# Kernel optimization log

Measured on AMD Instinct MI355X. Metric: run time of the kernel, lower is better.

Reference implementation:

```python
import jax, jax.numpy as jnp
import numpy as np

B, N, C, H = 2, 2048, 1024, 16
D = C // H
NEG = -1e9  # keras Softmax large negative for masked positions


def setup_inputs() -> dict:
    key = jax.random.key(0)
    ks = jax.random.split(key, 10)
    s = lambda fan_in: 1.0 / np.sqrt(fan_in)
    return {
        "x": jax.random.normal(ks[0], (B, N, C), jnp.float32),
        "mask": jnp.ones((B, 1, 1, N), jnp.bool_),
        "Wqkv": jax.random.normal(ks[1], (C, 3 * C), jnp.float32) * s(C),
        "bqkv": jnp.zeros((3 * C,), jnp.float32),
        "Wl": jax.random.normal(ks[2], (H, H), jnp.float32) * s(H),
        "bl": jnp.zeros((H,), jnp.float32),
        "Ww": jax.random.normal(ks[3], (H, H), jnp.float32) * s(H),
        "bw": jnp.zeros((H,), jnp.float32),
        "Wp": jax.random.normal(ks[4], (C, C), jnp.float32) * s(C),
        "bp": jnp.zeros((C,), jnp.float32),
    }


def reference(x, mask, Wqkv, bqkv, Wl, bl, Ww, bw, Wp, bp):
    scale = jnp.asarray(D ** -0.5, x.dtype)
    qkv = x @ Wqkv + bqkv                                  # [B,N,3C]
    qkv = qkv.reshape(B, N, 3, H, D).transpose(2, 0, 3, 1, 4)  # [3,B,H,N,D]
    q, k, v = qkv[0] * scale, qkv[1], qkv[2]
    attn = jnp.einsum("bhnd,bhmd->bhnm", q, k)             # [B,H,N,N]
    # pre-softmax talking-heads: mix head axis
    attn = jnp.einsum("bhnm,hg->bgnm", attn, Wl) + bl[None, :, None, None]
    # keras Softmax with boolean mask: add -1e9 where mask is False
    attn = attn + (1.0 - mask.astype(attn.dtype)) * NEG
    attn = jax.nn.softmax(attn, axis=-1)
    # post-softmax talking-heads
    attn = jnp.einsum("bhnm,hg->bgnm", attn, Ww) + bw[None, :, None, None]
    out = jnp.einsum("bhnm,bhmd->bhnd", attn, v)           # [B,H,N,D]
    out = out.transpose(0, 2, 1, 3).reshape(B, N, C)
    return out @ Wp + bp
```

## Files before the change

kernel.cpp:

```cpp
#include <hip/hip_runtime.h>
#include <hip/hip_bf16.h>


typedef __bf16 bf16_t;
typedef __bf16 bf16x8 __attribute__((ext_vector_type(8)));
typedef float f32x4 __attribute__((ext_vector_type(4)));

#define DEV static __device__ __forceinline__

static constexpr float NEGV = -1e9f;

DEV f32x4 mfma16(bf16x8 a, bf16x8 b, f32x4 c) {
  return __builtin_amdgcn_mfma_f32_16x16x32_bf16(a, b, c, 0, 0, 0);
}

DEV bf16x8 zero8() {
  bf16x8 z;
#pragma unroll
  for (int j = 0; j < 8; ++j) z[j] = (bf16_t)0.0f;
  return z;
}

DEV uint32_t pkbf(float lo, float hi) {
  union { bf16_t f; unsigned short s; } a, b;
  a.f = (bf16_t)lo; b.f = (bf16_t)hi;
  return (uint32_t)a.s | ((uint32_t)b.s << 16);
}

union U84 { uint32_t u[4]; bf16x8 v; };

__global__ __launch_bounds__(256) void mask_prep(const unsigned char* __restrict__ raw,
                                                 unsigned char* __restrict__ canon) {
  __shared__ int c0, c12;
  const int tid = threadIdx.x;
  if (tid == 0) { c0 = 0; c12 = 0; }
  __syncthreads();
  int l0 = 0, l12 = 0;
  for (int i = tid; i < 4096; i += 256) {
    unsigned char v = raw[i];
    if (v) {
      int r = i & 3;
      if (r == 0) l0++;
      else if (r < 3) l12++;
    }
  }
  if (l0) atomicAdd(&c0, l0);
  if (l12) atomicAdd(&c12, l12);
  __syncthreads();
  const int mode = (c0 == 0) ? 2 : ((c12 > 0) ? 0 : 1);
  for (int i = tid; i < 4096; i += 256) {
    bool t;
    if (mode == 0)      t = raw[i] != 0;
    else if (mode == 1) t = ((const int*)raw)[i] != 0;
    else                t = ((const float*)raw)[i] != 0.0f;
    canon[i] = t ? 1 : 0;
  }
}

__global__ __launch_bounds__(256) void gemm_kernel(
    const float* __restrict__ Af, const bf16_t* __restrict__ Ab,
    const float* __restrict__ Bw, const float* __restrict__ bias,
    float* __restrict__ outf,
    bf16_t* __restrict__ Qs, bf16_t* __restrict__ Ks, bf16_t* __restrict__ Vt,
    int K, int Nn, int epi) {
  __shared__ bf16_t As[64][40];
  __shared__ bf16_t Bs[64][40];
  const int tid = threadIdx.x;
  const int lane = tid & 63, wid = tid >> 6;
  const int bx = blockIdx.x, by = blockIdx.y;
  const int wr = (wid >> 1) * 32, wc = (wid & 1) * 32;
  const int lr = lane & 15, kq = lane >> 4;

  f32x4 acc[2][2];
#pragma unroll
  for (int i = 0; i < 2; ++i)
#pragma unroll
    for (int j = 0; j < 2; ++j) acc[i][j] = (f32x4){0.f, 0.f, 0.f, 0.f};

  for (int kt = 0; kt < K; kt += 32) {
    {
      const int row = tid >> 2, c8 = (tid & 3) * 8;
      if (epi == 0) {
        const float* p = Af + (size_t)(bx * 64 + row) * K + kt + c8;
        float4 v0 = *(const float4*)p;
        float4 v1 = *(const float4*)(p + 4);
        bf16x8 v;
        v[0] = (bf16_t)v0.x; v[1] = (bf16_t)v0.y; v[2] = (bf16_t)v0.z; v[3] = (bf16_t)v0.w;
        v[4] = (bf16_t)v1.x; v[5] = (bf16_t)v1.y; v[6] = (bf16_t)v1.z; v[7] = (bf16_t)v1.w;
        *(bf16x8*)&As[row][c8] = v;
      } else {
        *(bf16x8*)&As[row][c8] =
            *(const bf16x8*)(Ab + (size_t)(bx * 64 + row) * K + kt + c8);
      }
      const int krow = tid >> 3, n8 = (tid & 7) * 8;
      const float* bp = Bw + (size_t)(kt + krow) * Nn + by * 64 + n8;
      float4 b0 = *(const float4*)bp;
      float4 b1 = *(const float4*)(bp + 4);
      Bs[n8 + 0][krow] = (bf16_t)b0.x; Bs[n8 + 1][krow] = (bf16_t)b0.y;
      Bs[n8 + 2][krow] = (bf16_t)b0.z; Bs[n8 + 3][krow] = (bf16_t)b0.w;
      Bs[n8 + 4][krow] = (bf16_t)b1.x; Bs[n8 + 5][krow] = (bf16_t)b1.y;
      Bs[n8 + 6][krow] = (bf16_t)b1.z; Bs[n8 + 7][krow] = (bf16_t)b1.w;
    }
    __syncthreads();
#pragma unroll
    for (int rt = 0; rt < 2; ++rt) {
      bf16x8 af = *(const bf16x8*)&As[wr + rt * 16 + lr][kq * 8];
#pragma unroll
      for (int ct = 0; ct < 2; ++ct) {
        bf16x8 bf = *(const bf16x8*)&Bs[wc + ct * 16 + lr][kq * 8];
        acc[rt][ct] = mfma16(af, bf, acc[rt][ct]);
      }
    }
    __syncthreads();
  }

#pragma unroll
  for (int rt = 0; rt < 2; ++rt)
#pragma unroll
    for (int ct = 0; ct < 2; ++ct)
#pragma unroll
      for (int r = 0; r < 4; ++r) {
        const int grow = bx * 64 + wr + rt * 16 + kq * 4 + r;
        const int gcol = by * 64 + wc + ct * 16 + lr;
        const float v = acc[rt][ct][r] + bias[gcol];
        if (epi == 0) {
          const int t = gcol >> 10, h = (gcol >> 6) & 15, d = gcol & 63;
          const int b = grow >> 11, n = grow & 2047;
          if (t == 0)
            Qs[(((size_t)b * 16 + h) * 2048 + n) * 64 + d] = (bf16_t)(v * 0.125f);
          else if (t == 1)
            Ks[(((size_t)b * 16 + h) * 2048 + n) * 64 + d] = (bf16_t)v;
          else
            Vt[(((size_t)b * 16 + h) * 64 + d) * 2048 + n] = (bf16_t)v;
        } else {
          outf[(size_t)grow * Nn + gcol] = v;
        }
      }
}

__global__ __launch_bounds__(256) void vsum_kernel(const bf16_t* __restrict__ Vt,
                                                   float* __restrict__ Vsum) {
  const int lane = threadIdx.x & 63, wid = threadIdx.x >> 6;
  const int row = blockIdx.x * 4 + wid;
  const bf16_t* p = Vt + (size_t)row * 2048;
  float s = 0.f;
#pragma unroll
  for (int it = 0; it < 4; ++it) {
    bf16x8 v = *(const bf16x8*)(p + it * 512 + lane * 8);
#pragma unroll
    for (int j = 0; j < 8; ++j) s += (float)v[j];
  }
#pragma unroll
  for (int off = 32; off; off >>= 1) s += __shfl_xor(s, off);
  if (lane == 0) Vsum[row] = s;
}

__global__ __launch_bounds__(512, 4) void attn_pass1(
    const bf16_t* __restrict__ Qs, const bf16_t* __restrict__ Ks,
    const unsigned char* __restrict__ canon,
    const float* __restrict__ Wl, const float* __restrict__ bl,
    float2* __restrict__ pstats) {
  __shared__ uint32_t SE[512 * 10];
  const int tid = threadIdx.x, lane = tid & 63, wid = tid >> 6;
  const int g = lane & 15, kq = lane >> 4;
  const int b = blockIdx.z, n0 = blockIdx.x * 16, mbeg = blockIdx.y * 1024;
  const int h0 = wid * 2;

  bf16x8 wlf;
#pragma unroll
  for (int j = 0; j < 8; ++j) {
    const int k = kq * 8 + j;
    wlf[j] = (k < 16) ? (bf16_t)Wl[k * 16 + g] : (bf16_t)0.0f;
  }
  const float blg = bl[g];

  bf16x8 qf[2][2];
#pragma unroll
  for (int hh = 0; hh < 2; ++hh)
#pragma unroll
    for (int ks = 0; ks < 2; ++ks)
      qf[hh][ks] = *(const bf16x8*)(Qs + (((size_t)b * 16 + h0 + hh) * 2048 +
                                          n0 + g) * 64 + ks * 32 + kq * 8);

  float run_m[2] = {-3e38f, -3e38f}, run_l[2] = {0.f, 0.f};

  for (int m0 = mbeg; m0 < mbeg + 1024; m0 += 32) {
#pragma unroll
    for (int mt = 0; mt < 2; ++mt) {
      f32x4 a[2];
#pragma unroll
      for (int hh = 0; hh < 2; ++hh) {
        const bf16_t* kp = Ks + (((size_t)b * 16 + h0 + hh) * 2048 + m0 +
                                 mt * 16 + g) * 64 + kq * 8;
        a[hh] = mfma16(qf[hh][0], *(const bf16x8*)kp, (f32x4){0.f, 0.f, 0.f, 0.f});
        a[hh] = mfma16(qf[hh][1], *(const bf16x8*)(kp + 32), a[hh]);
      }
#pragma unroll
      for (int r = 0; r < 4; ++r) {
        const int p = (kq * 4 + r) * 32 + mt * 16 + g;
        SE[p * 10 + (wid ^ (kq & 1))] = pkbf(a[0][r], a[1][r]);
      }
    }
    __syncthreads();
#pragma unroll
    for (int pp = 0; pp < 4; ++pp) {
      const int pg = wid * 4 + pp, nl = pp >> 1, mt = pg & 1;
      const int prow = pg * 16 + g, bp = (prow >> 7) & 1;
      bf16x8 sf;
      if (kq < 2) {
        U84 t;
#pragma unroll
        for (int i = 0; i < 4; ++i) t.u[i] = SE[prow * 10 + ((kq * 4 + i) ^ bp)];
        sf = t.v;
      } else sf = zero8();
      f32x4 sp = mfma16(sf, wlf, (f32x4){blg, blg, blg, blg});
      const uchar4 mk = *(const uchar4*)(canon + b * 2048 + m0 + mt * 16 + kq * 4);
      if (!mk.x) sp[0] += NEGV;
      if (!mk.y) sp[1] += NEGV;
      if (!mk.z) sp[2] += NEGV;
      if (!mk.w) sp[3] += NEGV;
      float tm = fmaxf(fmaxf(sp[0], sp[1]), fmaxf(sp[2], sp[3]));
      tm = fmaxf(tm, __shfl_xor(tm, 16));
      tm = fmaxf(tm, __shfl_xor(tm, 32));
      const float nm = fmaxf(run_m[nl], tm);
      float s = __expf(sp[0] - nm) + __expf(sp[1] - nm) +
                __expf(sp[2] - nm) + __expf(sp[3] - nm);
      s += __shfl_xor(s, 16);
      s += __shfl_xor(s, 32);
      run_l[nl] = run_l[nl] * __expf(run_m[nl] - nm) + s;
      run_m[nl] = nm;
    }
    __syncthreads();
  }
  if (kq == 0) {
#pragma unroll
    for (int i = 0; i < 2; ++i) {
      const int n = n0 + wid * 2 + i;
      pstats[(((size_t)b * 2 + blockIdx.y) * 2048 + n) * 16 + g] =
          make_float2(run_m[i], run_l[i]);
    }
  }
}

__global__ __launch_bounds__(256) void stats_merge(const float2* __restrict__ ps,
                                                   float2* __restrict__ fin) {
  const int i = blockIdx.x * 256 + threadIdx.x;
  const int b = i >> 15, rest = i & 32767;
  const float2 p0 = ps[((size_t)b * 2 + 0) * 32768 + rest];
  const float2 p1 = ps[((size_t)b * 2 + 1) * 32768 + rest];
  const float M = fmaxf(p0.x, p1.x);
  const float L = p0.y * __expf(p0.x - M) + p1.y * __expf(p1.x - M);
  fin[i] = make_float2(M, 1.0f / L);
}

__global__ __launch_bounds__(512, 4) void attn_pass2(
    const bf16_t* __restrict__ Qs, const bf16_t* __restrict__ Ks,
    const bf16_t* __restrict__ Vt, const unsigned char* __restrict__ canon,
    const float* __restrict__ Wl, const float* __restrict__ bl,
    const float* __restrict__ Ww, const float2* __restrict__ fin2,
    float* __restrict__ Opart) {
  __shared__ uint32_t SE[512 * 10];
  __shared__ uint32_t Fw[16 * 324];
  const int tid = threadIdx.x, lane = tid & 63, wid = tid >> 6;
  const int g = lane & 15, kq = lane >> 4;
  const int b = blockIdx.z, n0 = blockIdx.x * 16, mbeg = blockIdx.y * 1024;
  const int h0 = wid * 2;

  bf16x8 wlf, wwt;
#pragma unroll
  for (int j = 0; j < 8; ++j) {
    const int k = kq * 8 + j;
    wlf[j] = (k < 16) ? (bf16_t)Wl[k * 16 + g] : (bf16_t)0.0f;
    wwt[j] = (k < 16) ? (bf16_t)Ww[k * 16 + g] : (bf16_t)0.0f;
  }
  f32x4 blv;
#pragma unroll
  for (int r = 0; r < 4; ++r) blv[r] = bl[kq * 4 + r];

  bf16x8 qf[2][2];
#pragma unroll
  for (int hh = 0; hh < 2; ++hh)
#pragma unroll
    for (int ks = 0; ks < 2; ++ks)
      qf[hh][ks] = *(const bf16x8*)(Qs + (((size_t)b * 16 + h0 + hh) * 2048 +
                                          n0 + g) * 64 + ks * 32 + kq * 8);

  f32x4 oacc[2][4];
#pragma unroll
  for (int i = 0; i < 2; ++i)
#pragma unroll
    for (int j = 0; j < 4; ++j) oacc[i][j] = (f32x4){0.f, 0.f, 0.f, 0.f};

  for (int m0 = mbeg; m0 < mbeg + 1024; m0 += 32) {
#pragma unroll
    for (int mt = 0; mt < 2; ++mt) {
      f32x4 a[2];
#pragma unroll
      for (int hh = 0; hh < 2; ++hh) {
        const bf16_t* kp = Ks + (((size_t)b * 16 + h0 + hh) * 2048 + m0 +
                                 mt * 16 + g) * 64 + kq * 8;
        a[hh] = mfma16(qf[hh][0], *(const bf16x8*)kp, (f32x4){0.f, 0.f, 0.f, 0.f});
        a[hh] = mfma16(qf[hh][1], *(const bf16x8*)(kp + 32), a[hh]);
      }
#pragma unroll
      for (int r = 0; r < 4; ++r) {
        const int p = (kq * 4 + r) * 32 + mt * 16 + g;
        SE[p * 10 + (wid ^ (kq & 1))] = pkbf(a[0][r], a[1][r]);
      }
    }
    __syncthreads();
#pragma unroll
    for (int pp = 0; pp < 4; ++pp) {
      const int pg = wid * 4 + pp, nl = pg >> 1, mt = pg & 1;
      const int prow = pg * 16 + g, bp = (prow >> 7) & 1;
      bf16x8 sf;
      if (kq < 2) {
        U84 t;
#pragma unroll
        for (int i = 0; i < 4; ++i) t.u[i] = SE[prow * 10 + ((kq * 4 + i) ^ bp)];
        sf = t.v;
      } else sf = zero8();
      f32x4 sp = mfma16(wlf, sf, blv);
      if (!canon[b * 2048 + m0 + mt * 16 + g]) {
        sp[0] += NEGV; sp[1] += NEGV; sp[2] += NEGV; sp[3] += NEGV;
      }
      const float4* st = (const float4*)((const float*)fin2 +
                          (((size_t)b * 2048 + n0 + nl) * 16 + kq * 4) * 2);
      const float4 s01 = st[0], s23 = st[1];
      const float e0 = __expf(sp[0] - s01.x) * s01.y;
      const float e1 = __expf(sp[1] - s01.z) * s01.w;
      const float e2 = __expf(sp[2] - s23.x) * s23.y;
      const float e3 = __expf(sp[3] - s23.z) * s23.w;
      uint2 ew;
      ew.x = pkbf(e0, e1);
      ew.y = pkbf(e2, e3);
      *(uint2*)&SE[prow * 10 + kq * 2] = ew;
      asm volatile("s_waitcnt lgkmcnt(0)" ::: "memory");
      __builtin_amdgcn_sched_barrier(0);
      bf16x8 ef;
      if (kq < 2) {
        U84 t;
#pragma unroll
        for (int i = 0; i < 4; ++i) t.u[i] = SE[prow * 10 + kq * 4 + i];
        ef = t.v;
      } else ef = zero8();
      f32x4 fp = mfma16(wwt, ef, (f32x4){0.f, 0.f, 0.f, 0.f});
      const int melem = mt * 16 + g;
      const int wm = (melem >> 1) ^ ((nl & 3) << 2);
#pragma unroll
      for (int r = 0; r < 4; ++r)
        ((bf16_t*)Fw)[(((kq * 4 + r) * 324) + nl * 20 + wm) * 2 + (melem & 1)] =
            (bf16_t)fp[r];
    }
    __syncthreads();
#pragma unroll
    for (int g2h = 0; g2h < 2; ++g2h) {
      const int g2 = h0 + g2h;
      bf16x8 af = *(const bf16x8*)&Fw[g2 * 324 + g * 20 + ((kq ^ (g & 3)) << 2)];
#pragma unroll
      for (int dt = 0; dt < 4; ++dt) {
        bf16x8 vf = *(const bf16x8*)(Vt + (((size_t)b * 16 + g2) * 64 + dt * 16 +
                                           g) * 2048 + m0 + kq * 8);
        oacc[g2h][dt] = mfma16(af, vf, oacc[g2h][dt]);
      }
    }
  }

#pragma unroll
  for (int g2h = 0; g2h < 2; ++g2h)
#pragma unroll
    for (int dt = 0; dt < 4; ++dt)
#pragma unroll
      for (int r = 0; r < 4; ++r) {
        const int n = n0 + kq * 4 + r;
        const int c = (h0 + g2h) * 64 + dt * 16 + g;
        Opart[(((size_t)b * 2 + blockIdx.y) * 2048 + n) * 1024 + c] =
            oacc[g2h][dt][r];
      }
}

__global__ __launch_bounds__(256) void reduce_ao(const float* __restrict__ Opart,
                                                 const float* __restrict__ bw,
                                                 const float* __restrict__ Vsum,
                                                 bf16_t* __restrict__ AO) {
  const size_t i = ((size_t)blockIdx.x * 256 + threadIdx.x) * 4;
  const int c = (int)(i & 1023), n = (int)((i >> 10) & 2047), b = (int)(i >> 21);
  const float4 p0 = *(const float4*)&Opart[(((size_t)b * 2 + 0) * 2048 + n) * 1024 + c];
  const float4 p1 = *(const float4*)&Opart[(((size_t)b * 2 + 1) * 2048 + n) * 1024 + c];
  float vv[4] = {p0.x + p1.x, p0.y + p1.y, p0.z + p1.z, p0.w + p1.w};
#pragma unroll
  for (int j = 0; j < 4; ++j) {
    const int cj = c + j, g2 = cj >> 6, d = cj & 63;
    AO[i + j] = (bf16_t)(vv[j] + bw[g2] * Vsum[((size_t)b * 16 + g2) * 64 + d]);
  }
}

extern "C" void kernel_launch(void* const* d_in, const int* in_sizes, int n_in,
                              void* d_out, int out_size, void* d_ws, size_t ws_size,
                              hipStream_t stream) {
  const float* x = (const float*)d_in[0];
  const unsigned char* mask = (const unsigned char*)d_in[1];
  const float* Wqkv = (const float*)d_in[2];
  const float* bqkv = (const float*)d_in[3];
  const float* Wl = (const float*)d_in[4];
  const float* bl = (const float*)d_in[5];
  const float* Ww = (const float*)d_in[6];
  const float* bw = (const float*)d_in[7];
  const float* Wp = (const float*)d_in[8];
  const float* bp = (const float*)d_in[9];
  float* out = (float*)d_out;

  char* w = (char*)d_ws;
  auto alloc = [&](size_t bytes) {
    char* p = w;
    w += (bytes + 255) & ~(size_t)255;
    return p;
  };
  bf16_t* Qs = (bf16_t*)alloc((size_t)2 * 16 * 2048 * 64 * 2);
  bf16_t* Ks = (bf16_t*)alloc((size_t)2 * 16 * 2048 * 64 * 2);
  bf16_t* Vt = (bf16_t*)alloc((size_t)2 * 16 * 2048 * 64 * 2);
  bf16_t* AO = (bf16_t*)alloc((size_t)4096 * 1024 * 2);
  float* Opart = (float*)alloc((size_t)4 * 2048 * 1024 * 4);
  float2* pstats = (float2*)alloc((size_t)2 * 2 * 2048 * 16 * 8);
  float2* fstats = (float2*)alloc((size_t)2 * 2048 * 16 * 8);
  float* Vsum = (float*)alloc((size_t)2048 * 4);
  unsigned char* canon = (unsigned char*)alloc(4096);

  mask_prep<<<dim3(1), dim3(256), 0, stream>>>(mask, canon);
  gemm_kernel<<<dim3(64, 48), dim3(256), 0, stream>>>(
      x, (const bf16_t*)nullptr, Wqkv, bqkv, nullptr, Qs, Ks, Vt, 1024, 3072, 0);
  vsum_kernel<<<dim3(512), dim3(256), 0, stream>>>(Vt, Vsum);
  attn_pass1<<<dim3(128, 2, 2), dim3(512), 0, stream>>>(Qs, Ks, canon, Wl, bl, pstats);
  stats_merge<<<dim3(256), dim3(256), 0, stream>>>(pstats, fstats);
  attn_pass2<<<dim3(128, 2, 2), dim3(512), 0, stream>>>(Qs, Ks, Vt, canon, Wl, bl, Ww,
                                                        fstats, Opart);
  reduce_ao<<<dim3(4096), dim3(256), 0, stream>>>(Opart, bw, Vsum, AO);
  gemm_kernel<<<dim3(64, 16), dim3(256), 0, stream>>>(
      (const float*)nullptr, AO, Wp, bp, out, nullptr, nullptr, nullptr, 1024, 1024, 1);
}
```

Baseline: 683.7 us.

## Fuse two-pass talking-heads attention into one kernel with unsplit key range

Replaces attn_pass1, stats_merge, attn_pass2 and reduce_ao with a single attn_fused kernel. Each block now covers the whole key range and walks it twice: once to accumulate softmax denominators, then again to compute normalized probabilities, the post-mix and the PV product, writing bf16 AO directly with the bw*Vsum term. This removes the large fp32 Opart round trip, the partial stats buffers and three launches. It also adds register double-buffering of K fragments and a per-batch all-true mask flag that skips per-element mask checks. The price is fewer blocks (256 of 512 threads) and softmax without subtracting the running max, which assumes logits stay small enough that exp does not overflow.

```diff
diff --git a/kernel.cpp b/kernel.cpp
--- a/kernel.cpp
+++ b/kernel.cpp
@@ -30,10 +30,11 @@
 union U84 { uint32_t u[4]; bf16x8 v; };
 
 __global__ __launch_bounds__(256) void mask_prep(const unsigned char* __restrict__ raw,
-                                                 unsigned char* __restrict__ canon) {
-  __shared__ int c0, c12;
+                                                 unsigned char* __restrict__ canon,
+                                                 unsigned char* __restrict__ allflag) {
+  __shared__ int c0, c12, f0, f1;
   const int tid = threadIdx.x;
-  if (tid == 0) { c0 = 0; c12 = 0; }
+  if (tid == 0) { c0 = 0; c12 = 0; f0 = 1; f1 = 1; }
   __syncthreads();
   int l0 = 0, l12 = 0;
   for (int i = tid; i < 4096; i += 256) {
@@ -54,7 +55,10 @@
     else if (mode == 1) t = ((const int*)raw)[i] != 0;
     else                t = ((const float*)raw)[i] != 0.0f;
     canon[i] = t ? 1 : 0;
-  }
+    if (!t) atomicAnd(i < 2048 ? &f0 : &f1, 0);
+  }
+  __syncthreads();
+  if (tid == 0) { allflag[0] = (unsigned char)f0; allflag[1] = (unsigned char)f1; }
 }
 
 __global__ __launch_bounds__(256) void gemm_kernel(
@@ -155,243 +159,206 @@
   if (lane == 0) Vsum[row] = s;
 }
 
-__global__ __launch_bounds__(512, 4) void attn_pass1(
+__global__ __launch_bounds__(512, 2) void attn_fused(
     const bf16_t* __restrict__ Qs, const bf16_t* __restrict__ Ks,
-    const unsigned char* __restrict__ canon,
+    const bf16_t* __restrict__ Vt, const unsigned char* __restrict__ canon,
+    const unsigned char* __restrict__ allflag,
     const float* __restrict__ Wl, const float* __restrict__ bl,
-    float2* __restrict__ pstats) {
-  __shared__ uint32_t SE[512 * 10];
+    const float* __restrict__ Ww, const float* __restrict__ bw,
+    const float* __restrict__ Vsum, bf16_t* __restrict__ AO) {
+  __shared__ uint32_t Sb[512 * 10];
+  __shared__ uint32_t Fb[16 * 324];
   const int tid = threadIdx.x, lane = tid & 63, wid = tid >> 6;
-  const int g = lane & 15, kq = lane >> 4;
-  const int b = blockIdx.z, n0 = blockIdx.x * 16, mbeg = blockIdx.y * 1024;
-  const int h0 = wid * 2;
-
-  bf16x8 wlf;
+  const int c = lane & 15, kq = lane >> 4;
+  const int id = blockIdx.x;
+  const int b = (id >> 2) & 1;
+  const int nt = ((id >> 3) << 2) | (id & 3);
+  const int n0 = nt * 16;
+  const int bh0 = b * 16 + 2 * wid;
+  const bool allt = allflag[b] != 0;
+
+  bf16x8 wlf, wwf;
 #pragma unroll
   for (int j = 0; j < 8; ++j) {
     const int k = kq * 8 + j;
-    wlf[j] = (k < 16) ? (bf16_t)Wl[k * 16 + g] : (bf16_t)0.0f;
-  }
-  const float blg = bl[g];
+    wlf[j] = (k < 16) ? (bf16_t)Wl[k * 16 + c] : (bf16_t)0.0f;
+    wwf[j] = (k < 16) ? (bf16_t)Ww[k * 16 + c] : (bf16_t)0.0f;
+  }
+  f32x4 blv;
+#pragma unroll
+  for (int r = 0; r < 4; ++r) blv[r] = bl[kq * 4 + r];
 
   bf16x8 qf[2][2];
 #pragma unroll
   for (int hh = 0; hh < 2; ++hh)
 #pragma unroll
     for (int ks = 0; ks < 2; ++ks)
-      qf[hh][ks] = *(const bf16x8*)(Qs + (((size_t)b * 16 + h0 + hh) * 2048 +
-                                          n0 + g) * 64 + ks * 32 + kq * 8);
-
-  float run_m[2] = {-3e38f, -3e38f}, run_l[2] = {0.f, 0.f};
-
-  for (int m0 = mbeg; m0 < mbeg + 1024; m0 += 32) {
+      qf[hh][ks] = *(const bf16x8*)(Qs + ((size_t)(bh0 + hh) * 2048 + n0 + c) * 64 +
+                                    ks * 32 + kq * 8);
+
+  struct KF { bf16x8 f[2][2][2]; };
+  auto loadK = [&](int v) {
+    KF k;
+    const int m0 = (v < 64 ? v : 63) * 32;
+#pragma unroll
+    for (int hh = 0; hh < 2; ++hh)
+#pragma unroll
+      for (int mt = 0; mt < 2; ++mt)
+#pragma unroll
+        for (int ks = 0; ks < 2; ++ks)
+          k.f[hh][mt][ks] = *(const bf16x8*)(Ks + ((size_t)(bh0 + hh) * 2048 + m0 +
+                                                   mt * 16 + c) * 64 + ks * 32 + kq * 8);
+    return k;
+  };
+
+  auto stage = [&](const KF& k) {
 #pragma unroll
     for (int mt = 0; mt < 2; ++mt) {
-      f32x4 a[2];
-#pragma unroll
-      for (int hh = 0; hh < 2; ++hh) {
-        const bf16_t* kp = Ks + (((size_t)b * 16 + h0 + hh) * 2048 + m0 +
-                                 mt * 16 + g) * 64 + kq * 8;
-        a[hh] = mfma16(qf[hh][0], *(const bf16x8*)kp, (f32x4){0.f, 0.f, 0.f, 0.f});
-        a[hh] = mfma16(qf[hh][1], *(const bf16x8*)(kp + 32), a[hh]);
-      }
+      f32x4 a0 = (f32x4){0.f, 0.f, 0.f, 0.f};
+      f32x4 a1 = (f32x4){0.f, 0.f, 0.f, 0.f};
+      a0 = mfma16(qf[0][0], k.f[0][mt][0], a0);
+      a0 = mfma16(qf[0][1], k.f[0][mt][1], a0);
+      a1 = mfma16(qf[1][0], k.f[1][mt][0], a1);
+      a1 = mfma16(qf[1][1], k.f[1][mt][1], a1);
 #pragma unroll
       for (int r = 0; r < 4; ++r) {
-        const int p = (kq * 4 + r) * 32 + mt * 16 + g;
-        SE[p * 10 + (wid ^ (kq & 1))] = pkbf(a[0][r], a[1][r]);
-      }
-    }
-    __syncthreads();
-#pragma unroll
-    for (int pp = 0; pp < 4; ++pp) {
-      const int pg = wid * 4 + pp, nl = pp >> 1, mt = pg & 1;
-      const int prow = pg * 16 + g, bp = (prow >> 7) & 1;
-      bf16x8 sf;
-      if (kq < 2) {
-        U84 t;
-#pragma unroll
-        for (int i = 0; i < 4; ++i) t.u[i] = SE[prow * 10 + ((kq * 4 + i) ^ bp)];
-        sf = t.v;
-      } else sf = zero8();
-      f32x4 sp = mfma16(sf, wlf, (f32x4){blg, blg, blg, blg});
-      const uchar4 mk = *(const uchar4*)(canon + b * 2048 + m0 + mt * 16 + kq * 4);
-      if (!mk.x) sp[0] += NEGV;
-      if (!mk.y) sp[1] += NEGV;
-      if (!mk.z) sp[2] += NEGV;
-      if (!mk.w) sp[3] += NEGV;
-      float tm = fmaxf(fmaxf(sp[0], sp[1]), fmaxf(sp[2], sp[3]));
-      tm = fmaxf(tm, __shfl_xor(tm, 16));
-      tm = fmaxf(tm, __shfl_xor(tm, 32));
-      const float nm = fmaxf(run_m[nl], tm);
-      float s = __expf(sp[0] - nm) + __expf(sp[1] - nm) +
-                __expf(sp[2] - nm) + __expf(sp[3] - nm);
-      s += __shfl_xor(s, 16);
-      s += __shfl_xor(s, 32);
-      run_l[nl] = run_l[nl] * __expf(run_m[nl] - nm) + s;
-      run_m[nl] = nm;
-    }
-    __syncthreads();
-  }
-  if (kq == 0) {
-#pragma unroll
-    for (int i = 0; i < 2; ++i) {
-      const int n = n0 + wid * 2 + i;
-      pstats[(((size_t)b * 2 + blockIdx.y) * 2048 + n) * 16 + g] =
-          make_float2(run_m[i], run_l[i]);
-    }
-  }
-}
-
-__global__ __launch_bounds__(256) void stats_merge(const float2* __restrict__ ps,
-                                                   float2* __restrict__ fin) {
-  const int i = blockIdx.x * 256 + threadIdx.x;
-  const int b = i >> 15, rest = i & 32767;
-  const float2 p0 = ps[((size_t)b * 2 + 0) * 32768 + rest];
-  const float2 p1 = ps[((size_t)b * 2 + 1) * 32768 + rest];
-  const float M = fmaxf(p0.x, p1.x);
-  const float L = p0.y * __expf(p0.x - M) + p1.y * __expf(p1.x - M);
-  fin[i] = make_float2(M, 1.0f / L);
-}
-
-__global__ __launch_bounds__(512, 4) void attn_pass2(
-    const bf16_t* __restrict__ Qs, const bf16_t* __restrict__ Ks,
-    const bf16_t* __restrict__ Vt, const unsigned char* __restrict__ canon,
-    const float* __restrict__ Wl, const float* __restrict__ bl,
-    const float* __restrict__ Ww, const float2* __restrict__ fin2,
-    float* __restrict__ Opart) {
-  __shared__ uint32_t SE[512 * 10];
-  __shared__ uint32_t Fw[16 * 324];
-  const int tid = threadIdx.x, lane = tid & 63, wid = tid >> 6;
-  const int g = lane & 15, kq = lane >> 4;
-  const int b = blockIdx.z, n0 = blockIdx.x * 16, mbeg = blockIdx.y * 1024;
-  const int h0 = wid * 2;
-
-  bf16x8 wlf, wwt;
-#pragma unroll
-  for (int j = 0; j < 8; ++j) {
-    const int k = kq * 8 + j;
-    wlf[j] = (k < 16) ? (bf16_t)Wl[k * 16 + g] : (bf16_t)0.0f;
-    wwt[j] = (k < 16) ? (bf16_t)Ww[k * 16 + g] : (bf16_t)0.0f;
-  }
-  f32x4 blv;
-#pragma unroll
-  for (int r = 0; r < 4; ++r) blv[r] = bl[kq * 4 + r];
-
-  bf16x8 qf[2][2];
-#pragma unroll
-  for (int hh = 0; hh < 2; ++hh)
-#pragma unroll
-    for (int ks = 0; ks < 2; ++ks)
-      qf[hh][ks] = *(const bf16x8*)(Qs + (((size_t)b * 16 + h0 + hh) * 2048 +
-                                          n0 + g) * 64 + ks * 32 + kq * 8);
+        const int p = (kq * 4 + r) * 32 + mt * 16 + c;
+        Sb[p * 10 + (wid ^ (kq & 1))] = pkbf(a0[r], a1[r]);
+      }
+    }
+  };
+
+  auto gatherS = [&](int pp) {
+    const int prow = (wid * 4 + pp) * 16 + c;
+    const int bp = (prow >> 7) & 1;
+    if (kq < 2) {
+      U84 t;
+#pragma unroll
+      for (int i = 0; i < 4; ++i) t.u[i] = Sb[prow * 10 + ((kq * 4 + i) ^ bp)];
+      return t.v;
+    }
+    return zero8();
+  };
+
+  float lacc[4][2];
+#pragma unroll
+  for (int r = 0; r < 4; ++r) { lacc[r][0] = 0.f; lacc[r][1] = 0.f; }
+  {
+    KF kf = loadK(0);
+    for (int u = 0; u < 64; ++u) {
+      stage(kf);
+      kf = loadK(u + 1);
+      __syncthreads();
+#pragma unroll
+      for (int pp = 0; pp < 4; ++pp) {
+        bf16x8 sf = gatherS(pp);
+        f32x4 d1 = mfma16(wlf, sf, blv);
+        if (!allt && !canon[b * 2048 + u * 32 + (pp & 1) * 16 + c]) {
+          d1[0] += NEGV; d1[1] += NEGV; d1[2] += NEGV; d1[3] += NEGV;
+        }
+        const int ns = pp >> 1;
+#pragma unroll
+        for (int r = 0; r < 4; ++r) lacc[r][ns] += __expf(d1[r]);
+      }
+      __syncthreads();
+    }
+  }
+  float invl[4][2];
+#pragma unroll
+  for (int r = 0; r < 4; ++r)
+#pragma unroll
+    for (int ns = 0; ns < 2; ++ns) {
+      float s = lacc[r][ns];
+      s += __shfl_xor(s, 1);
+      s += __shfl_xor(s, 2);
+      s += __shfl_xor(s, 4);
+      s += __shfl_xor(s, 8);
+      invl[r][ns] = 1.0f / s;
+    }
 
   f32x4 oacc[2][4];
 #pragma unroll
   for (int i = 0; i < 2; ++i)
 #pragma unroll
     for (int j = 0; j < 4; ++j) oacc[i][j] = (f32x4){0.f, 0.f, 0.f, 0.f};
-
-  for (int m0 = mbeg; m0 < mbeg + 1024; m0 += 32) {
-#pragma unroll
-    for (int mt = 0; mt < 2; ++mt) {
-      f32x4 a[2];
-#pragma unroll
-      for (int hh = 0; hh < 2; ++hh) {
-        const bf16_t* kp = Ks + (((size_t)b * 16 + h0 + hh) * 2048 + m0 +
-                                 mt * 16 + g) * 64 + kq * 8;
-        a[hh] = mfma16(qf[hh][0], *(const bf16x8*)kp, (f32x4){0.f, 0.f, 0.f, 0.f});
-        a[hh] = mfma16(qf[hh][1], *(const bf16x8*)(kp + 32), a[hh]);
-      }
-#pragma unroll
-      for (int r = 0; r < 4; ++r) {
-        const int p = (kq * 4 + r) * 32 + mt * 16 + g;
-        SE[p * 10 + (wid ^ (kq & 1))] = pkbf(a[0][r], a[1][r]);
-      }
-    }
-    __syncthreads();
-#pragma unroll
-    for (int pp = 0; pp < 4; ++pp) {
-      const int pg = wid * 4 + pp, nl = pg >> 1, mt = pg & 1;
-      const int prow = pg * 16 + g, bp = (prow >> 7) & 1;
-      bf16x8 sf;
-      if (kq < 2) {
-        U84 t;
-#pragma unroll
-        for (int i = 0; i < 4; ++i) t.u[i] = SE[prow * 10 + ((kq * 4 + i) ^ bp)];
-        sf = t.v;
-      } else sf = zero8();
-      f32x4 sp = mfma16(wlf, sf, blv);
-      if (!canon[b * 2048 + m0 + mt * 16 + g]) {
-        sp[0] += NEGV; sp[1] += NEGV; sp[2] += NEGV; sp[3] += NEGV;
-      }
-      const float4* st = (const float4*)((const float*)fin2 +
-                          (((size_t)b * 2048 + n0 + nl) * 16 + kq * 4) * 2);
-      const float4 s01 = st[0], s23 = st[1];
-      const float e0 = __expf(sp[0] - s01.x) * s01.y;
-      const float e1 = __expf(sp[1] - s01.z) * s01.w;
-      const float e2 = __expf(sp[2] - s23.x) * s23.y;
-      const float e3 = __expf(sp[3] - s23.z) * s23.w;
-      uint2 ew;
-      ew.x = pkbf(e0, e1);
-      ew.y = pkbf(e2, e3);
-      *(uint2*)&SE[prow * 10 + kq * 2] = ew;
+  {
+    KF kf = loadK(0);
+    for (int u = 0; u < 64; ++u) {
+      stage(kf);
+      kf = loadK(u + 1);
+      __syncthreads();
+      bf16x8 vr[2][4];
+#pragma unroll
+      for (int g2h = 0; g2h < 2; ++g2h)
+#pragma unroll
+        for (int dt = 0; dt < 4; ++dt)
+          vr[g2h][dt] = *(const bf16x8*)(Vt + ((size_t)(bh0 + g2h) * 64 + dt * 16 + c) *
+                                                  2048 + u * 32 + kq * 8);
+#pragma unroll
+      for (int pp = 0; pp < 4; ++pp) {
+        bf16x8 sf = gatherS(pp);
+        f32x4 d1 = mfma16(wlf, sf, blv);
+        if (!allt && !canon[b * 2048 + u * 32 + (pp & 1) * 16 + c]) {
+          d1[0] += NEGV; d1[1] += NEGV; d1[2] += NEGV; d1[3] += NEGV;
+        }
+        const int ns = pp >> 1;
+        const float e0 = __expf(d1[0]) * invl[0][ns];
+        const float e1 = __expf(d1[1]) * invl[1][ns];
+        const float e2 = __expf(d1[2]) * invl[2][ns];
+        const float e3 = __expf(d1[3]) * invl[3][ns];
+        const int prow = (wid * 4 + pp) * 16 + c;
+        uint2 ew;
+        ew.x = pkbf(e0, e1);
+        ew.y = pkbf(e2, e3);
+        *(uint2*)&Sb[prow * 10 + kq * 2] = ew;
+      }
       asm volatile("s_waitcnt lgkmcnt(0)" ::: "memory");
       __builtin_amdgcn_sched_barrier(0);
-      bf16x8 ef;
-      if (kq < 2) {
-        U84 t;
-#pragma unroll
-        for (int i = 0; i < 4; ++i) t.u[i] = SE[prow * 10 + kq * 4 + i];
-        ef = t.v;
-      } else ef = zero8();
-      f32x4 fp = mfma16(wwt, ef, (f32x4){0.f, 0.f, 0.f, 0.f});
-      const int melem = mt * 16 + g;
-      const int wm = (melem >> 1) ^ ((nl & 3) << 2);
-#pragma unroll
-      for (int r = 0; r < 4; ++r)
-        ((bf16_t*)Fw)[(((kq * 4 + r) * 324) + nl * 20 + wm) * 2 + (melem & 1)] =
-            (bf16_t)fp[r];
-    }
-    __syncthreads();
-#pragma unroll
-    for (int g2h = 0; g2h < 2; ++g2h) {
-      const int g2 = h0 + g2h;
-      bf16x8 af = *(const bf16x8*)&Fw[g2 * 324 + g * 20 + ((kq ^ (g & 3)) << 2)];
-#pragma unroll
-      for (int dt = 0; dt < 4; ++dt) {
-        bf16x8 vf = *(const bf16x8*)(Vt + (((size_t)b * 16 + g2) * 64 + dt * 16 +
-                                           g) * 2048 + m0 + kq * 8);
-        oacc[g2h][dt] = mfma16(af, vf, oacc[g2h][dt]);
-      }
-    }
-  }
-
-#pragma unroll
-  for (int g2h = 0; g2h < 2; ++g2h)
-#pragma unroll
-    for (int dt = 0; dt < 4; ++dt)
+#pragma unroll
+      for (int pp = 0; pp < 4; ++pp) {
+        const int pg = wid * 4 + pp;
+        const int prow = pg * 16 + c;
+        bf16x8 ef;
+        if (kq < 2) {
+          U84 t;
+#pragma unroll
+          for (int i = 0; i < 4; ++i) t.u[i] = Sb[prow * 10 + kq * 4 + i];
+          ef = t.v;
+        } else ef = zero8();
+        f32x4 d2 = mfma16(wwf, ef, (f32x4){0.f, 0.f, 0.f, 0.f});
+        const int nl = pg >> 1, ml = (pg & 1) * 16 + c;
+        const int wm = (ml >> 1) ^ ((nl & 3) << 2);
+#pragma unroll
+        for (int r = 0; r < 4; ++r)
+          ((bf16_t*)Fb)[(((kq * 4 + r) * 324) + nl * 20 + wm) * 2 + (ml & 1)] =
+              (bf16_t)d2[r];
+      }
+      __syncthreads();
+#pragma unroll
+      for (int g2h = 0; g2h < 2; ++g2h) {
+        bf16x8 af = *(const bf16x8*)&Fb[(2 * wid + g2h) * 324 + c * 20 +
+                                        ((kq ^ (c & 3)) << 2)];
+#pragma unroll
+        for (int dt = 0; dt < 4; ++dt)
+          oacc[g2h][dt] = mfma16(af, vr[g2h][dt], oacc[g2h][dt]);
+      }
+    }
+  }
+
+#pragma unroll
+  for (int g2h = 0; g2h < 2; ++g2h) {
+    const int g2 = 2 * wid + g2h;
+    const float bwv = bw[g2];
+#pragma unroll
+    for (int dt = 0; dt < 4; ++dt) {
+      const float vs = Vsum[(size_t)(b * 16 + g2) * 64 + dt * 16 + c];
 #pragma unroll
       for (int r = 0; r < 4; ++r) {
         const int n = n0 + kq * 4 + r;
-        const int c = (h0 + g2h) * 64 + dt * 16 + g;
-        Opart[(((size_t)b * 2 + blockIdx.y) * 2048 + n) * 1024 + c] =
-            oacc[g2h][dt][r];
-      }
-}
-
-__global__ __launch_bounds__(256) void reduce_ao(const float* __restrict__ Opart,
-                                                 const float* __restrict__ bw,
-                                                 const float* __restrict__ Vsum,
-                                                 bf16_t* __restrict__ AO) {
-  const size_t i = ((size_t)blockIdx.x * 256 + threadIdx.x) * 4;
-  const int c = (int)(i & 1023), n = (int)((i >> 10) & 2047), b = (int)(i >> 21);
-  const float4 p0 = *(const float4*)&Opart[(((size_t)b * 2 + 0) * 2048 + n) * 1024 + c];
-  const float4 p1 = *(const float4*)&Opart[(((size_t)b * 2 + 1) * 2048 + n) * 1024 + c];
-  float vv[4] = {p0.x + p1.x, p0.y + p1.y, p0.z + p1.z, p0.w + p1.w};
-#pragma unroll
-  for (int j = 0; j < 4; ++j) {
-    const int cj = c + j, g2 = cj >> 6, d = cj & 63;
-    AO[i + j] = (bf16_t)(vv[j] + bw[g2] * Vsum[((size_t)b * 16 + g2) * 64 + d]);
+        AO[((size_t)b * 2048 + n) * 1024 + g2 * 64 + dt * 16 + c] =
+            (bf16_t)(oacc[g2h][dt][r] + bwv * vs);
+      }
+    }
   }
 }
 
@@ -420,21 +387,16 @@
   bf16_t* Ks = (bf16_t*)alloc((size_t)2 * 16 * 2048 * 64 * 2);
   bf16_t* Vt = (bf16_t*)alloc((size_t)2 * 16 * 2048 * 64 * 2);
   bf16_t* AO = (bf16_t*)alloc((size_t)4096 * 1024 * 2);
-  float* Opart = (float*)alloc((size_t)4 * 2048 * 1024 * 4);
-  float2* pstats = (float2*)alloc((size_t)2 * 2 * 2048 * 16 * 8);
-  float2* fstats = (float2*)alloc((size_t)2 * 2048 * 16 * 8);
   float* Vsum = (float*)alloc((size_t)2048 * 4);
   unsigned char* canon = (unsigned char*)alloc(4096);
-
-  mask_prep<<<dim3(1), dim3(256), 0, stream>>>(mask, canon);
+  unsigned char* allflag = (unsigned char*)alloc(256);
+
+  mask_prep<<<dim3(1), dim3(256), 0, stream>>>(mask, canon, allflag);
   gemm_kernel<<<dim3(64, 48), dim3(256), 0, stream>>>(
       x, (const bf16_t*)nullptr, Wqkv, bqkv, nullptr, Qs, Ks, Vt, 1024, 3072, 0);
   vsum_kernel<<<dim3(512), dim3(256), 0, stream>>>(Vt, Vsum);
-  attn_pass1<<<dim3(128, 2, 2), dim3(512), 0, stream>>>(Qs, Ks, canon, Wl, bl, pstats);
-  stats_merge<<<dim3(256), dim3(256), 0, stream>>>(pstats, fstats);
-  attn_pass2<<<dim3(128, 2, 2), dim3(512), 0, stream>>>(Qs, Ks, Vt, canon, Wl, bl, Ww,
-                                                        fstats, Opart);
-  reduce_ao<<<dim3(4096), dim3(256), 0, stream>>>(Opart, bw, Vsum, AO);
+  attn_fused<<<dim3(256), dim3(512), 0, stream>>>(Qs, Ks, Vt, canon, allflag, Wl, bl,
+                                                  Ww, bw, Vsum, AO);
   gemm_kernel<<<dim3(64, 16), dim3(256), 0, stream>>>(
       (const float*)nullptr, AO, Wp, bp, out, nullptr, nullptr, nullptr, 1024, 1024, 1);
 }
```

Result: faster. 567.4 us (-17.0%).
